# Kernel tuning notes

Measured on AMD Instinct MI355X. Metric: run time of the kernel, lower is better.

The kernel has to match this reference:

```python
import jax, jax.numpy as jnp
import numpy as np

B, L, D, H, W = 2, 1024, 1024, 16, 64  # batch, length, dim, num_head, band_width
DH = D // H  # head_dim = 64


def setup_inputs() -> dict:
    key = jax.random.key(0)
    ks = jax.random.split(key, 7)
    scale = 0.02
    return {
        "x": jax.random.normal(ks[0], (B, L, D), dtype=jnp.float32),
        "Wq": jax.random.normal(ks[1], (D, D), dtype=jnp.float32) * scale,
        "Wk": jax.random.normal(ks[2], (D, D), dtype=jnp.float32) * scale,
        "Wv": jax.random.normal(ks[3], (D, D), dtype=jnp.float32) * scale,
        "Wo": jax.random.normal(ks[4], (D, D), dtype=jnp.float32) * scale,
        "last_k_init": jax.random.normal(ks[5], (W - 1, H, DH), dtype=jnp.float32),
        "last_v_init": jax.random.normal(ks[6], (W - 1, H, DH), dtype=jnp.float32),
    }


def reference(x, Wq, Wk, Wv, Wo, last_k_init, last_v_init):
    b, l, d = x.shape
    w1, h, dh = last_k_init.shape  # band_width-1, num_head, head_dim
    w = w1 + 1

    # torch nn.Linear: y = x @ W.T (no bias)
    q = (x @ Wq.T).reshape(b, l, h, dh)
    k = (x @ Wk.T).reshape(b, l, h, dh)
    v = (x @ Wv.T).reshape(b, l, h, dh)

    # prepend learned initial cache (fresh state: last_k is None)
    last_k = jnp.broadcast_to(last_k_init[None], (b, w1, h, dh))
    last_v = jnp.broadcast_to(last_v_init[None], (b, w1, h, dh))
    k_pad = jnp.concatenate([last_k, k], axis=1)  # [b, l+w-1, h, dh]
    v_pad = jnp.concatenate([last_v, v], axis=1)

    # query at position t attends offsets i in [0, w): key index t + i in padded
    # array == original position t - (w-1) + i  (causal sliding window of width w)
    idx = jnp.arange(l)[:, None] + jnp.arange(w)[None, :]  # [l, w]
    k_win = k_pad[:, idx]  # [b, l, w, h, dh]
    v_win = v_pad[:, idx]  # [b, l, w, h, dh]

    scores = jnp.einsum('blhd,blwhd->blwh', q, k_win) * (dh ** -0.5)
    attn = jax.nn.softmax(scores, axis=2)  # softmax over band offsets
    out = jnp.einsum('blwh,blwhd->blhd', attn, v_win).reshape(b, l, d)
    return out @ Wo.T
```

## Files before the change

### kernel.cpp

```cpp
#include <hip/hip_runtime.h>
#include <hip/hip_bf16.h>
#include <stdint.h>

#define B_ 2
#define L_ 1024
#define D_ 1024
#define H_ 16
#define W_ 64
#define DH_ 64
#define BK 64

typedef __attribute__((ext_vector_type(8))) __bf16 bf16x8;
typedef __attribute__((ext_vector_type(4))) float floatx4;

#define AS3(p) ((__attribute__((address_space(3))) void*)(p))
#define AS1(p) ((const __attribute__((address_space(1))) void*)(p))

static __device__ __forceinline__ ushort f2bf(float f) {
    union { float f; uint32_t u; } v{f};
    uint32_t r = v.u + 0x7fff + ((v.u >> 16) & 1);
    return (ushort)(r >> 16);
}
static __device__ __forceinline__ uint32_t pack2(float a, float b) {
    return (uint32_t)f2bf(a) | ((uint32_t)f2bf(b) << 16);
}

__global__ __launch_bounds__(256) void cvt_inputs(
    const float* __restrict__ x, const float* __restrict__ wq, const float* __restrict__ wk,
    const float* __restrict__ wv, const float* __restrict__ wo,
    ushort* __restrict__ xb, ushort* __restrict__ wqb, ushort* __restrict__ wkb,
    ushort* __restrict__ wvb, ushort* __restrict__ wob) {
    const size_t M1 = 1u << 20;
    size_t i4 = ((size_t)blockIdx.x * 256 + threadIdx.x) * 4;
    const float* s; ushort* d; size_t off;
    if (i4 < 2 * M1)      { s = x;  d = xb;  off = i4; }
    else if (i4 < 3 * M1) { s = wq; d = wqb; off = i4 - 2 * M1; }
    else if (i4 < 4 * M1) { s = wk; d = wkb; off = i4 - 3 * M1; }
    else if (i4 < 5 * M1) { s = wv; d = wvb; off = i4 - 4 * M1; }
    else                  { s = wo; d = wob; off = i4 - 5 * M1; }
    float4 f = *(const float4*)(s + off);
    ushort4 o;
    o.x = f2bf(f.x); o.y = f2bf(f.y); o.z = f2bf(f.z); o.w = f2bf(f.w);
    *(ushort4*)(d + off) = o;
}

__global__ __launch_bounds__(256, 6) void gemm_qkv(
    const ushort* __restrict__ xb,
    const ushort* __restrict__ wqb, const ushort* __restrict__ wkb, const ushort* __restrict__ wvb,
    ushort* __restrict__ q, ushort* __restrict__ k, ushort* __restrict__ v) {
    __shared__ __align__(16) ushort As[64 * BK];
    __shared__ __align__(16) ushort Bs[64 * BK];
    const int tid = threadIdx.x;
    const int m0 = blockIdx.x * 64;
    const int nt = blockIdx.y;
    const int which = nt >> 4;
    const int n0 = (nt & 15) * 64;
    const ushort* wsel = which == 0 ? wqb : (which == 1 ? wkb : wvb);
    ushort* dsel = which == 0 ? q : (which == 1 ? k : v);

    const int lane = tid & 63;
    const int wv_ = tid >> 6;
    const int wm = wv_ * 16;
    const int lr = lane & 15;
    const int quad = lane >> 4;

    floatx4 acc[4];
#pragma unroll
    for (int j = 0; j < 4; ++j) acc[j] = (floatx4){0.f, 0.f, 0.f, 0.f};

    int offA[2], offB[2];
#pragma unroll
    for (int it = 0; it < 2; ++it) {
        int c = tid + it * 256;
        int r = c >> 3, s = c & 7, g = s ^ (r & 7);
        offA[it] = (m0 + r) * 1024 + g * 8;
        offB[it] = (n0 + r) * 1024 + g * 8;
    }

    for (int k0 = 0; k0 < 1024; k0 += BK) {
#pragma unroll
        for (int it = 0; it < 2; ++it)
            __builtin_amdgcn_global_load_lds(AS1(xb + offA[it] + k0), AS3(As + (it * 256 + tid) * 8), 16, 0, 0);
#pragma unroll
        for (int it = 0; it < 2; ++it)
            __builtin_amdgcn_global_load_lds(AS1(wsel + offB[it] + k0), AS3(Bs + (it * 256 + tid) * 8), 16, 0, 0);
        __syncthreads();
#pragma unroll
        for (int ks = 0; ks < 2; ++ks) {
            int ra = wm + lr;
            bf16x8 af = *(const bf16x8*)(As + ra * BK + (((ks * 4 + quad) ^ (ra & 7)) * 8));
            bf16x8 bfr[4];
#pragma unroll
            for (int j = 0; j < 4; ++j) {
                int r = j * 16 + lr;
                bfr[j] = *(const bf16x8*)(Bs + r * BK + (((ks * 4 + quad) ^ (r & 7)) * 8));
            }
#pragma unroll
            for (int j = 0; j < 4; ++j)
                acc[j] = __builtin_amdgcn_mfma_f32_16x16x32_bf16(af, bfr[j], acc[j], 0, 0, 0);
        }
        __syncthreads();
    }

#pragma unroll
    for (int j = 0; j < 4; ++j) {
        int c = n0 + j * 16 + lr;
        int h = c >> 6, dh = c & 63;
#pragma unroll
        for (int r = 0; r < 4; ++r) {
            int m = m0 + wm + quad * 4 + r;
            int bb = m >> 10, l = m & 1023;
            dsel[(((size_t)bb * 16 + h) * 1024 + l) * 64 + dh] = f2bf(acc[j][r]);
        }
    }
}

__global__ __launch_bounds__(256) void gemm_wo(
    const ushort* __restrict__ ab,
    const ushort* __restrict__ wob,
    float* __restrict__ out) {
    __shared__ __align__(16) ushort As[64 * BK];
    __shared__ __align__(16) ushort Bs[64 * BK];
    const int tid = threadIdx.x;
    const int m0 = blockIdx.x * 64;
    const int n0 = blockIdx.y * 64;
    const int lane = tid & 63;
    const int wv_ = tid >> 6;
    const int wm = wv_ * 16;
    const int lr = lane & 15;
    const int quad = lane >> 4;

    floatx4 acc[4];
#pragma unroll
    for (int j = 0; j < 4; ++j) acc[j] = (floatx4){0.f, 0.f, 0.f, 0.f};

    int offA[2], offB[2];
#pragma unroll
    for (int it = 0; it < 2; ++it) {
        int c = tid + it * 256;
        int r = c >> 3, s = c & 7, g = s ^ (r & 7);
        offA[it] = (m0 + r) * 1024 + g * 8;
        offB[it] = (n0 + r) * 1024 + g * 8;
    }

    for (int k0 = 0; k0 < 1024; k0 += BK) {
#pragma unroll
        for (int it = 0; it < 2; ++it)
            __builtin_amdgcn_global_load_lds(AS1(ab + offA[it] + k0), AS3(As + (it * 256 + tid) * 8), 16, 0, 0);
#pragma unroll
        for (int it = 0; it < 2; ++it)
            __builtin_amdgcn_global_load_lds(AS1(wob + offB[it] + k0), AS3(Bs + (it * 256 + tid) * 8), 16, 0, 0);
        __syncthreads();
#pragma unroll
        for (int ks = 0; ks < 2; ++ks) {
            int ra = wm + lr;
            bf16x8 af = *(const bf16x8*)(As + ra * BK + (((ks * 4 + quad) ^ (ra & 7)) * 8));
            bf16x8 bfr[4];
#pragma unroll
            for (int j = 0; j < 4; ++j) {
                int r = j * 16 + lr;
                bfr[j] = *(const bf16x8*)(Bs + r * BK + (((ks * 4 + quad) ^ (r & 7)) * 8));
            }
#pragma unroll
            for (int j = 0; j < 4; ++j)
                acc[j] = __builtin_amdgcn_mfma_f32_16x16x32_bf16(af, bfr[j], acc[j], 0, 0, 0);
        }
        __syncthreads();
    }

#pragma unroll
    for (int j = 0; j < 4; ++j) {
        int c = n0 + j * 16 + lr;
#pragma unroll
        for (int r = 0; r < 4; ++r) {
            int m = m0 + wm + quad * 4 + r;
            out[(size_t)m * 1024 + c] = acc[j][r];
        }
    }
}

#define STRQ 72
#define STRV 136

__global__ __launch_bounds__(256) void band_attn3(
    const ushort* __restrict__ q,
    const ushort* __restrict__ k,
    const ushort* __restrict__ v,
    const float* __restrict__ lastk,
    const float* __restrict__ lastv,
    ushort* __restrict__ ao) {
    __shared__ __align__(16) ushort Qs[64 * STRQ];
    __shared__ __align__(16) ushort Kw[128 * STRQ];
    __shared__ __align__(16) ushort Vt[64 * STRV];
    __shared__ __align__(16) ushort Ps[64 * STRV];
    const int tid = threadIdx.x;
    const int lane = tid & 63;
    const int wid = tid >> 6;
    const int l0 = blockIdx.x * 64;
    const int b = blockIdx.y >> 4, h = blockIdx.y & 15;
    const size_t hb = (size_t)(b * 16 + h) * 1024 * 64;

#pragma unroll
    for (int it = 0; it < 2; ++it) {
        int c = tid + it * 256;
        int rr = c >> 3, cc = (c & 7) * 8;
        *(uint4*)(Qs + rr * STRQ + cc) = *(const uint4*)(q + hb + (size_t)(l0 + rr) * 64 + cc);
    }
#pragma unroll
    for (int it = 0; it < 4; ++it) {
        int c = tid + it * 256;
        int j = c >> 3, cc = (c & 7) * 8;
        int pos = l0 + j - 63;
        uint4 t = {0u, 0u, 0u, 0u};
        if (j < 127) {
            if (pos >= 0) {
                t = *(const uint4*)(k + hb + (size_t)pos * 64 + cc);
            } else {
                const float* sk = lastk + ((size_t)j * 16 + h) * 64 + cc;
                float4 a0 = *(const float4*)sk, a1 = *(const float4*)(sk + 4);
                t.x = pack2(a0.x, a0.y); t.y = pack2(a0.z, a0.w);
                t.z = pack2(a1.x, a1.y); t.w = pack2(a1.z, a1.w);
            }
        }
        *(uint4*)(Kw + j * STRQ + cc) = t;
    }
#pragma unroll
    for (int it = 0; it < 4; ++it) {
        int c = tid + it * 256;
        int j = c >> 3, d8 = (c & 7) * 8;
        int pos = l0 + j - 63;
        ushort tv[8];
        if (j >= 127) {
#pragma unroll
            for (int t = 0; t < 8; ++t) tv[t] = 0;
        } else if (pos >= 0) {
            union { uint4 u4; ushort us[8]; } tu;
            tu.u4 = *(const uint4*)(v + hb + (size_t)pos * 64 + d8);
#pragma unroll
            for (int t = 0; t < 8; ++t) tv[t] = tu.us[t];
        } else {
            const float* sv = lastv + ((size_t)j * 16 + h) * 64 + d8;
#pragma unroll
            for (int t = 0; t < 8; ++t) tv[t] = f2bf(sv[t]);
        }
#pragma unroll
        for (int t = 0; t < 8; ++t) Vt[(size_t)(d8 + t) * STRV + j] = tv[t];
    }
    __syncthreads();

    const int lr = lane & 15;
    const int quad = lane >> 4;

    floatx4 sa[8];
#pragma unroll
    for (int nt = 0; nt < 8; ++nt) sa[nt] = (floatx4){0.f, 0.f, 0.f, 0.f};
    bf16x8 aq[2];
#pragma unroll
    for (int ks = 0; ks < 2; ++ks)
        aq[ks] = *(const bf16x8*)(Qs + (wid * 16 + lr) * STRQ + ks * 32 + quad * 8);
#pragma unroll
    for (int ks = 0; ks < 2; ++ks)
#pragma unroll
        for (int nt = 0; nt < 8; ++nt) {
            bf16x8 bk = *(const bf16x8*)(Kw + (nt * 16 + lr) * STRQ + ks * 32 + quad * 8);
            sa[nt] = __builtin_amdgcn_mfma_f32_16x16x32_bf16(aq[ks], bk, sa[nt], 0, 0, 0);
        }

#pragma unroll
    for (int rr = 0; rr < 4; ++rr) {
        int i_loc = wid * 16 + quad * 4 + rr;
        float svv[8];
        float mv = -1e30f;
#pragma unroll
        for (int nt = 0; nt < 8; ++nt) {
            int j = nt * 16 + lr;
            int w = j - i_loc;
            svv[nt] = (w >= 0 && w < 64) ? sa[nt][rr] * 0.125f : -1e30f;
            mv = fmaxf(mv, svv[nt]);
        }
#pragma unroll
        for (int off = 8; off; off >>= 1) mv = fmaxf(mv, __shfl_xor(mv, off, 16));
        float sum = 0.f;
#pragma unroll
        for (int nt = 0; nt < 8; ++nt) {
            svv[nt] = __expf(svv[nt] - mv);
            sum += svv[nt];
        }
#pragma unroll
        for (int off = 8; off; off >>= 1) sum += __shfl_xor(sum, off, 16);
        float inv = 1.f / sum;
#pragma unroll
        for (int nt = 0; nt < 8; ++nt)
            Ps[(size_t)i_loc * STRV + nt * 16 + lr] = f2bf(svv[nt] * inv);
    }

    floatx4 oa[4];
#pragma unroll
    for (int nt = 0; nt < 4; ++nt) oa[nt] = (floatx4){0.f, 0.f, 0.f, 0.f};
#pragma unroll
    for (int ks = 0; ks < 4; ++ks) {
        bf16x8 ap = *(const bf16x8*)(Ps + (wid * 16 + lr) * STRV + ks * 32 + quad * 8);
#pragma unroll
        for (int nt = 0; nt < 4; ++nt) {
            bf16x8 bv = *(const bf16x8*)(Vt + (nt * 16 + lr) * STRV + ks * 32 + quad * 8);
            oa[nt] = __builtin_amdgcn_mfma_f32_16x16x32_bf16(ap, bv, oa[nt], 0, 0, 0);
        }
    }

#pragma unroll
    for (int nt = 0; nt < 4; ++nt) {
        int d = nt * 16 + lr;
#pragma unroll
        for (int rr = 0; rr < 4; ++rr) {
            int i_loc = wid * 16 + quad * 4 + rr;
            ao[((size_t)b * 1024 + l0 + i_loc) * 1024 + h * 64 + d] = f2bf(oa[nt][rr]);
        }
    }
}

extern "C" void kernel_launch(void* const* d_in, const int* in_sizes, int n_in,
                              void* d_out, int out_size, void* d_ws, size_t ws_size,
                              hipStream_t stream) {
    const float* x     = (const float*)d_in[0];
    const float* Wq    = (const float*)d_in[1];
    const float* Wk    = (const float*)d_in[2];
    const float* Wv    = (const float*)d_in[3];
    const float* Wo    = (const float*)d_in[4];
    const float* lastk = (const float*)d_in[5];
    const float* lastv = (const float*)d_in[6];
    float* out = (float*)d_out;

    const size_t M1 = 1u << 20;
    ushort* xb  = (ushort*)d_ws;
    ushort* wqb = xb + 2 * M1;
    ushort* wkb = wqb + M1;
    ushort* wvb = wkb + M1;
    ushort* wob = wvb + M1;
    ushort* qh  = wob + M1;
    ushort* kh  = qh + 2 * M1;
    ushort* vh  = kh + 2 * M1;
    ushort* ao  = vh + 2 * M1;

    cvt_inputs<<<6144, 256, 0, stream>>>(x, Wq, Wk, Wv, Wo, xb, wqb, wkb, wvb, wob);
    gemm_qkv<<<dim3(32, 48), 256, 0, stream>>>(xb, wqb, wkb, wvb, qh, kh, vh);
    band_attn3<<<dim3(16, 32), 256, 0, stream>>>(qh, kh, vh, lastk, lastv, ao);
    gemm_wo<<<dim3(32, 16), 256, 0, stream>>>(ao, wob, out);
}
```

Measured before the change: 122.5 us.

## Fuse Q/K/V projections into one block sharing the x tile

Each block now computes the same 64x64 output tile for all three projections (Q, K, V), loading the x tile into shared memory once and reusing it across three weight tiles. This cuts redundant x loads and triples the MFMA work per block, while the grid shrinks from 1536 to 512 blocks. In exchange it uses more shared memory and accumulator registers (48 floats per thread), drops the occupancy hint, and leaves fewer blocks to spread across CUs.

```diff
diff --git a/kernel.cpp b/kernel.cpp
--- a/kernel.cpp
+++ b/kernel.cpp
@@ -44,19 +44,17 @@
     *(ushort4*)(d + off) = o;
 }
 
-__global__ __launch_bounds__(256, 6) void gemm_qkv(
+__global__ __launch_bounds__(256) void gemm_qkv3(
     const ushort* __restrict__ xb,
     const ushort* __restrict__ wqb, const ushort* __restrict__ wkb, const ushort* __restrict__ wvb,
     ushort* __restrict__ q, ushort* __restrict__ k, ushort* __restrict__ v) {
     __shared__ __align__(16) ushort As[64 * BK];
-    __shared__ __align__(16) ushort Bs[64 * BK];
+    __shared__ __align__(16) ushort Bs[3][64 * BK];
     const int tid = threadIdx.x;
-    const int m0 = blockIdx.x * 64;
-    const int nt = blockIdx.y;
-    const int which = nt >> 4;
-    const int n0 = (nt & 15) * 64;
-    const ushort* wsel = which == 0 ? wqb : (which == 1 ? wkb : wvb);
-    ushort* dsel = which == 0 ? q : (which == 1 ? k : v);
+    const int n0 = blockIdx.x * 64;
+    const int m0 = blockIdx.y * 64;
+    const ushort* wsel[3] = {wqb, wkb, wvb};
+    ushort* dsel[3] = {q, k, v};
 
     const int lane = tid & 63;
     const int wv_ = tid >> 6;
@@ -64,9 +62,11 @@
     const int lr = lane & 15;
     const int quad = lane >> 4;
 
-    floatx4 acc[4];
-#pragma unroll
-    for (int j = 0; j < 4; ++j) acc[j] = (floatx4){0.f, 0.f, 0.f, 0.f};
+    floatx4 acc[3][4];
+#pragma unroll
+    for (int w3 = 0; w3 < 3; ++w3)
+#pragma unroll
+        for (int j = 0; j < 4; ++j) acc[w3][j] = (floatx4){0.f, 0.f, 0.f, 0.f};
 
     int offA[2], offB[2];
 #pragma unroll
@@ -82,35 +82,43 @@
         for (int it = 0; it < 2; ++it)
             __builtin_amdgcn_global_load_lds(AS1(xb + offA[it] + k0), AS3(As + (it * 256 + tid) * 8), 16, 0, 0);
 #pragma unroll
-        for (int it = 0; it < 2; ++it)
-            __builtin_amdgcn_global_load_lds(AS1(wsel + offB[it] + k0), AS3(Bs + (it * 256 + tid) * 8), 16, 0, 0);
+        for (int w3 = 0; w3 < 3; ++w3)
+#pragma unroll
+            for (int it = 0; it < 2; ++it)
+                __builtin_amdgcn_global_load_lds(AS1(wsel[w3] + offB[it] + k0), AS3(Bs[w3] + (it * 256 + tid) * 8), 16, 0, 0);
         __syncthreads();
 #pragma unroll
         for (int ks = 0; ks < 2; ++ks) {
             int ra = wm + lr;
             bf16x8 af = *(const bf16x8*)(As + ra * BK + (((ks * 4 + quad) ^ (ra & 7)) * 8));
-            bf16x8 bfr[4];
-#pragma unroll
-            for (int j = 0; j < 4; ++j) {
-                int r = j * 16 + lr;
-                bfr[j] = *(const bf16x8*)(Bs + r * BK + (((ks * 4 + quad) ^ (r & 7)) * 8));
+#pragma unroll
+            for (int w3 = 0; w3 < 3; ++w3) {
+                bf16x8 bfr[4];
+#pragma unroll
+                for (int j = 0; j < 4; ++j) {
+                    int r = j * 16 + lr;
+                    bfr[j] = *(const bf16x8*)(Bs[w3] + r * BK + (((ks * 4 + quad) ^ (r & 7)) * 8));
+                }
+#pragma unroll
+                for (int j = 0; j < 4; ++j)
+                    acc[w3][j] = __builtin_amdgcn_mfma_f32_16x16x32_bf16(af, bfr[j], acc[w3][j], 0, 0, 0);
             }
-#pragma unroll
-            for (int j = 0; j < 4; ++j)
-                acc[j] = __builtin_amdgcn_mfma_f32_16x16x32_bf16(af, bfr[j], acc[j], 0, 0, 0);
         }
         __syncthreads();
     }
 
 #pragma unroll
-    for (int j = 0; j < 4; ++j) {
-        int c = n0 + j * 16 + lr;
-        int h = c >> 6, dh = c & 63;
-#pragma unroll
-        for (int r = 0; r < 4; ++r) {
-            int m = m0 + wm + quad * 4 + r;
-            int bb = m >> 10, l = m & 1023;
-            dsel[(((size_t)bb * 16 + h) * 1024 + l) * 64 + dh] = f2bf(acc[j][r]);
+    for (int w3 = 0; w3 < 3; ++w3) {
+#pragma unroll
+        for (int j = 0; j < 4; ++j) {
+            int c = n0 + j * 16 + lr;
+            int h = c >> 6, dh = c & 63;
+#pragma unroll
+            for (int r = 0; r < 4; ++r) {
+                int m = m0 + wm + quad * 4 + r;
+                int bb = m >> 10, l = m & 1023;
+                dsel[w3][(((size_t)bb * 16 + h) * 1024 + l) * 64 + dh] = f2bf(acc[w3][j][r]);
+            }
         }
     }
 }
@@ -342,7 +350,7 @@
     ushort* ao  = vh + 2 * M1;
 
     cvt_inputs<<<6144, 256, 0, stream>>>(x, Wq, Wk, Wv, Wo, xb, wqb, wkb, wvb, wob);
-    gemm_qkv<<<dim3(32, 48), 256, 0, stream>>>(xb, wqb, wkb, wvb, qh, kh, vh);
+    gemm_qkv3<<<dim3(16, 32), 256, 0, stream>>>(xb, wqb, wkb, wvb, qh, kh, vh);
     band_attn3<<<dim3(16, 32), 256, 0, stream>>>(qh, kh, vh, lastk, lastv, ao);
     gemm_wo<<<dim3(32, 16), 256, 0, stream>>>(ao, wob, out);
 }
```

Result: slower. 125.0 us (+2.1%).
